# Kernel tuning notes

Hardware: AMD Instinct MI355X
Metric: run time of the kernel (lower is better)

The kernel has to match this reference:

```python
import jax, jax.numpy as jnp
import numpy as np

N_NODES = 100000
N_EDGES = 1000000
D = 64  # gat_input_size == gat_hidden_size
NEG_SLOPE = 0.2  # PyG GATConv default leaky_relu slope


def setup_inputs() -> dict:
    key = jax.random.key(0)
    k1, k2, k3, k4, k5, k6 = jax.random.split(key, 6)
    g = jax.random.normal(k1, (N_NODES, D), dtype=jnp.float32)
    edge_index = jax.random.randint(k2, (2, N_EDGES), 0, N_NODES, dtype=jnp.int32)
    scale = 1.0 / np.sqrt(D)
    W = jax.random.normal(k3, (D, D), dtype=jnp.float32) * scale
    att_src = jax.random.normal(k4, (D,), dtype=jnp.float32) * scale
    att_dst = jax.random.normal(k5, (D,), dtype=jnp.float32) * scale
    bias = jnp.zeros((D,), dtype=jnp.float32)
    return {"g": g, "edge_index": edge_index, "W": W,
            "att_src": att_src, "att_dst": att_dst, "bias": bias}


def _gat_layer(x, src, dst, W, att_src, att_dst, bias):
    N = x.shape[0]
    h = x @ W                               # [N, D] projected features
    a_src = h @ att_src                     # [N] per-node source logits
    a_dst = h @ att_dst                     # [N] per-node target logits
    e = jax.nn.leaky_relu(a_src[src] + a_dst[dst], NEG_SLOPE)  # [E]
    # numerically stable segment softmax over edges grouped by target node
    m = jax.ops.segment_max(e, dst, num_segments=N)            # [N]
    m = jnp.where(jnp.isfinite(m), m, 0.0)                     # isolated nodes
    ex = jnp.exp(e - m[dst])                                   # [E]
    denom = jax.ops.segment_sum(ex, dst, num_segments=N)       # [N]
    alpha = ex / (denom[dst] + 1e-16)                          # [E]
    out = jax.ops.segment_sum(alpha[:, None] * h[src], dst, num_segments=N)
    return out + bias


def reference(g, edge_index, W, att_src, att_dst, bias):
    src, dst = edge_index[0], edge_index[1]
    for _ in range(4):  # same shared GAT applied 4 times
        g = _gat_layer(g, src, dst, W, att_src, att_dst, bias)
    return g
```

## Files before the change

### kernel.cpp

```cpp
#include <hip/hip_runtime.h>
#include <hip/hip_bf16.h>

typedef unsigned int u32;
typedef unsigned short u16;
typedef unsigned long long u64;
typedef __attribute__((ext_vector_type(8))) short short8;
typedef __attribute__((ext_vector_type(4))) float f32x4;

#define LRELU_SLOPE 0.2f
#define BPB 32
#define MAXPER 13000

__device__ inline float bfbits(u32 hi) { union { u32 i; float f; } v; v.i = hi; return v.f; }
__device__ inline float bflo(u32 w) { return bfbits(w << 16); }
__device__ inline float bfhi(u32 w) { return bfbits(w & 0xFFFF0000u); }
__device__ inline float bf2f(u16 s) { return bfbits(((u32)s) << 16); }
__device__ inline u16 f2bf(float f) {
  union { float f; u32 i; } v; v.f = f;
  u32 r = v.i + 0x7FFFu + ((v.i >> 16) & 1u);
  return (u16)(r >> 16);
}

__global__ void detect_kernel(const u32* __restrict__ g, int nwords, int* __restrict__ mode) {
  __shared__ int cnt;
  if (threadIdx.x == 0) cnt = 0;
  __syncthreads();
  int c = 0;
  for (int i = threadIdx.x; i < nwords; i += blockDim.x) {
    u32 e = g[i] & 0x7F80u;
    if (e >= 0x3000u && e <= 0x4180u) c++;
  }
  atomicAdd(&cnt, c);
  __syncthreads();
  if (threadIdx.x == 0) *mode = (2 * cnt > nwords) ? 1 : 0;
}

__global__ void conv_x_kernel(const void* __restrict__ g, u16* __restrict__ x, int n,
                              const int* __restrict__ mode) {
  if (*mode) return;
  int i = blockIdx.x * blockDim.x + threadIdx.x;
  if (i >= n) return;
  x[i] = f2bf(((const float*)g)[i]);
}

__global__ void params_kernel(const void* __restrict__ W, const void* __restrict__ as,
                              const void* __restrict__ ad, const void* __restrict__ bs,
                              float* __restrict__ pf, u16* __restrict__ wfrag,
                              const int* __restrict__ mode) {
  int md = *mode;
  for (int i = threadIdx.x; i < 4288; i += 256) {
    const void* p; int j;
    if (i < 4096)      { p = W;  j = i; }
    else if (i < 4160) { p = as; j = i - 4096; }
    else if (i < 4224) { p = ad; j = i - 4160; }
    else               { p = bs; j = i - 4224; }
    pf[i] = md ? bf2f(((const u16*)p)[j]) : ((const float*)p)[j];
  }
  __syncthreads();
  for (int i = threadIdx.x; i < 4096; i += 256) {
    int f = i >> 9, lane = (i >> 3) & 63, j = i & 7;
    int c = f >> 1, t = f & 1;
    int k = 32 * t + 8 * (lane >> 4) + j;
    int n = 16 * c + (lane & 15);
    wfrag[i] = f2bf(pf[k * 64 + n]);
  }
}

__global__ void __launch_bounds__(256) binA_kernel(
    const int* __restrict__ src, const int* __restrict__ dst, int* __restrict__ gcnt,
    uint2* __restrict__ binned, int E, int nper, int cap) {
  __shared__ int lcnt[8], lbase[8], lcur[8];
  const int K = 8;
  int tile0 = blockIdx.x * (256 * K);
  int t = threadIdx.x;
  if (t < 8) { lcnt[t] = 0; lcur[t] = 0; }
  __syncthreads();
  int dv[K], sv[K], bv[K];
#pragma unroll
  for (int j = 0; j < K; ++j) {
    int idx = tile0 + j * 256 + t;
    bool ok = idx < E;
    int d = ok ? __builtin_nontemporal_load(&dst[idx]) : 0;
    int s = ok ? __builtin_nontemporal_load(&src[idx]) : 0;
    int b = -1;
    if (ok) {
      b = (d >= 4 * nper) ? 4 : 0;
      if (d >= (b + 2) * nper) b += 2;
      if (d >= (b + 1) * nper) b += 1;
      atomicAdd(&lcnt[b], 1);
    }
    dv[j] = d; sv[j] = s; bv[j] = b;
  }
  __syncthreads();
  if (t < 8) lbase[t] = atomicAdd(&gcnt[t], lcnt[t]);
  __syncthreads();
#pragma unroll
  for (int j = 0; j < K; ++j) {
    int b = bv[j];
    if (b >= 0) {
      int slot = lbase[b] + atomicAdd(&lcur[b], 1);
      if (slot < cap) binned[(size_t)b * cap + slot] = make_uint2((u32)sv[j], (u32)dv[j]);
    }
  }
}

__global__ void __launch_bounds__(256) histA_kernel(
    const uint2* __restrict__ binned, const int* __restrict__ gcnt,
    u32* __restrict__ slices, int nper, int cap) {
  __shared__ u32 cnt_lds[MAXPER];
  int b = blockIdx.x & 7;
  int j = blockIdx.x >> 3;
  int cnt = gcnt[b]; if (cnt > cap) cnt = cap;
  int chunk = (cnt + BPB - 1) / BPB;
  int begin = j * chunk;
  int endc = begin + chunk; if (endc > cnt) endc = cnt;
  for (int k = threadIdx.x; k < nper; k += 256) cnt_lds[k] = 0;
  __syncthreads();
  const uint2* reg = binned + (size_t)b * cap;
  int kbase = b * nper;
  for (int i = begin + threadIdx.x; i < endc; i += 256)
    atomicAdd(&cnt_lds[(int)reg[i].y - kbase], 1u);
  __syncthreads();
  u32* out = slices + (size_t)(b * BPB + j) * nper;
  for (int k = threadIdx.x; k < nper; k += 256) out[k] = cnt_lds[k];
}

__global__ void reduce_deg_kernel(const u32* __restrict__ slices, int* __restrict__ deg,
                                  int nper, int N) {
  int b = blockIdx.x & 7;
  int kk = (blockIdx.x >> 3) * blockDim.x + threadIdx.x;
  if (kk >= nper) return;
  int k = b * nper + kk;
  if (k >= N) return;
  const u32* s = slices + (size_t)b * BPB * nper + kk;
  u32 t = 0;
#pragma unroll 8
  for (int j = 0; j < BPB; ++j) t += s[(size_t)j * nper];
  deg[k] = (int)t;
}

__global__ void base_kernel(u32* __restrict__ slices, const int* __restrict__ row_off,
                            int nper, int N) {
  int b = blockIdx.x & 7;
  int kk = (blockIdx.x >> 3) * blockDim.x + threadIdx.x;
  if (kk >= nper) return;
  int k = b * nper + kk;
  if (k >= N) return;
  u32 run = (u32)row_off[k];
  u32* s = slices + (size_t)b * BPB * nper + kk;
#pragma unroll 8
  for (int j = 0; j < BPB; ++j) {
    u32 t = s[(size_t)j * nper];
    s[(size_t)j * nper] = run;
    run += t;
  }
}

__global__ void __launch_bounds__(256) scatterB_kernel(
    const uint2* __restrict__ binned, const int* __restrict__ gcnt,
    const u32* __restrict__ slices, int* __restrict__ csr_src, int nper, int cap) {
  __shared__ u32 base_lds[MAXPER];
  int b = blockIdx.x & 7;
  int j = blockIdx.x >> 3;
  int cnt = gcnt[b]; if (cnt > cap) cnt = cap;
  int chunk = (cnt + BPB - 1) / BPB;
  int begin = j * chunk;
  int endc = begin + chunk; if (endc > cnt) endc = cnt;
  const u32* s = slices + (size_t)(b * BPB + j) * nper;
  for (int k = threadIdx.x; k < nper; k += 256) base_lds[k] = s[k];
  __syncthreads();
  const uint2* reg = binned + (size_t)b * cap;
  int kbase = b * nper;
  for (int i = begin + threadIdx.x; i < endc; i += 256) {
    uint2 r = reg[i];
    u32 p = atomicAdd(&base_lds[(int)r.y - kbase], 1u);
    csr_src[p] = (int)r.x;
  }
}

__global__ void hist_local_kernel(const uint2* __restrict__ binned, const int* __restrict__ gcnt,
                                  int* __restrict__ deg, int cap) {
  int b = blockIdx.x & 7;
  int vb = blockIdx.x >> 3, nvb = gridDim.x >> 3;
  int cnt = gcnt[b]; if (cnt > cap) cnt = cap;
  const uint2* reg = binned + (size_t)b * cap;
  for (int i = vb * blockDim.x + threadIdx.x; i < cnt; i += nvb * blockDim.x)
    atomicAdd(&deg[reg[i].y], 1);
}

__global__ void scatter_local_kernel(const uint2* __restrict__ binned, const int* __restrict__ gcnt,
                                     int* __restrict__ cursor, int* __restrict__ csr_src, int cap) {
  int b = blockIdx.x & 7;
  int vb = blockIdx.x >> 3, nvb = gridDim.x >> 3;
  int cnt = gcnt[b]; if (cnt > cap) cnt = cap;
  const uint2* reg = binned + (size_t)b * cap;
  for (int i = vb * blockDim.x + threadIdx.x; i < cnt; i += nvb * blockDim.x) {
    uint2 r = reg[i];
    int p = atomicAdd(&cursor[r.y], 1);
    csr_src[p] = (int)r.x;
  }
}

__global__ void scan1_kernel(const int* __restrict__ deg, int* __restrict__ row_off,
                             int* __restrict__ partials, int N) {
  __shared__ int smem[1024];
  int t = threadIdx.x;
  int idx = blockIdx.x * 1024 + t;
  int v = (idx < N) ? deg[idx] : 0;
  smem[t] = v;
  __syncthreads();
  for (int off = 1; off < 1024; off <<= 1) {
    int u = (t >= off) ? smem[t - off] : 0;
    __syncthreads();
    smem[t] += u;
    __syncthreads();
  }
  if (idx < N) row_off[idx + 1] = smem[t];
  if (t == 1023) partials[blockIdx.x] = smem[t];
}

__global__ void scan2_kernel(int* __restrict__ partials, int P) {
  __shared__ int smem[1024];
  int t = threadIdx.x;
  int v = (t < P) ? partials[t] : 0;
  smem[t] = v;
  __syncthreads();
  for (int off = 1; off < 1024; off <<= 1) {
    int u = (t >= off) ? smem[t - off] : 0;
    __syncthreads();
    smem[t] += u;
    __syncthreads();
  }
  if (t < P) partials[t] = smem[t];
}

__global__ void scan3_kernel(int* __restrict__ row_off, const int* __restrict__ partials,
                             int* __restrict__ cursor, int N) {
  int b = blockIdx.x;
  int idx = b * 1024 + threadIdx.x;
  if (idx < N) {
    int v = row_off[idx + 1] + ((b > 0) ? partials[b - 1] : 0);
    row_off[idx + 1] = v;
    if (idx + 1 < N) cursor[idx + 1] = v;
  }
  if (idx == 0) { row_off[0] = 0; cursor[0] = 0; }
}

__global__ void __launch_bounds__(256) proj_mfma_kernel(
    const u16* __restrict__ x, const void* __restrict__ graw, const int* __restrict__ mode,
    int first, const u16* __restrict__ wfrag, const float* __restrict__ pf,
    u16* __restrict__ h, float* __restrict__ a_src, float* __restrict__ a_dst, int N) {
  int lane = threadIdx.x & 63;
  int quad = lane >> 4, m = lane & 15;
  int wtile = (int)((blockIdx.x * (size_t)blockDim.x + threadIdx.x) >> 6);
  int ntiles = (N + 15) >> 4;
  int nwaves = (int)((gridDim.x * (size_t)blockDim.x) >> 6);

  const u16* xin = (first && *mode) ? (const u16*)graw : x;

  short8 bfrag[8];
#pragma unroll
  for (int f = 0; f < 8; ++f)
    bfrag[f] = *(const short8*)(wfrag + f * 512 + lane * 8);
  float asv[4], adv[4];
#pragma unroll
  for (int c = 0; c < 4; ++c) {
    asv[c] = pf[4096 + 16 * c + m];
    adv[c] = pf[4160 + 16 * c + m];
  }

  for (int tile = wtile; tile < ntiles; tile += nwaves) {
    int row0 = tile << 4;
    int rl = row0 + m; if (rl > N - 1) rl = N - 1;
    const u16* xr = xin + (size_t)rl * 64 + 8 * quad;
    short8 a0 = *(const short8*)(xr);
    short8 a1 = *(const short8*)(xr + 32);

    f32x4 acc[4];
#pragma unroll
    for (int c = 0; c < 4; ++c) {
      f32x4 z = {0.f, 0.f, 0.f, 0.f};
      z = __builtin_amdgcn_mfma_f32_16x16x32_bf16(a0, bfrag[2 * c + 0], z, 0, 0, 0);
      z = __builtin_amdgcn_mfma_f32_16x16x32_bf16(a1, bfrag[2 * c + 1], z, 0, 0, 0);
      acc[c] = z;
    }

#pragma unroll
    for (int r = 0; r < 4; ++r) {
      int row = row0 + 4 * quad + r;
      float v0 = acc[0][r], v1 = acc[1][r], v2 = acc[2][r], v3 = acc[3][r];
      if (row < N) {
        u16* hr = h + (size_t)row * 64 + m;
        hr[0]  = f2bf(v0);
        hr[16] = f2bf(v1);
        hr[32] = f2bf(v2);
        hr[48] = f2bf(v3);
      }
      float s1 = v0 * asv[0] + v1 * asv[1] + v2 * asv[2] + v3 * asv[3];
      float s2 = v0 * adv[0] + v1 * adv[1] + v2 * adv[2] + v3 * adv[3];
#pragma unroll
      for (int msk = 1; msk <= 8; msk <<= 1) {
        s1 += __shfl_xor(s1, msk, 64);
        s2 += __shfl_xor(s2, msk, 64);
      }
      if (m == 0 && row < N) { a_src[row] = s1; a_dst[row] = s2; }
    }
  }
}

__global__ void __launch_bounds__(256) gather_kernel(
    const u16* __restrict__ h, const float* __restrict__ a_src,
    const float* __restrict__ a_dst, const int* __restrict__ row_off,
    const int* __restrict__ csr_src, const float* __restrict__ pf,
    u16* __restrict__ xout, void* __restrict__ dout, int N, int last,
    const int* __restrict__ mode) {
  int lane = threadIdx.x & 63;
  int grp = lane >> 4;
  int eg  = (lane >> 3) & 1;
  int fg  = lane & 7;
  int wid = (int)((blockIdx.x * blockDim.x + threadIdx.x) >> 6);
  int i0 = wid * 4;
  if (i0 >= N) return;
  int i = i0 + grp;
  bool valid = i < N;

  int beg = 0, end = 0;
  float adv = 0.f;
  if (valid) {
    beg = row_off[i];
    end = row_off[i + 1];
    adv = a_dst[i];
  }

  float acc[8] = {0.f, 0.f, 0.f, 0.f, 0.f, 0.f, 0.f, 0.f};
  float den = 0.f;

  if (beg < end) {
    int lastE = end - 1;
    for (int b0 = beg; b0 < end; b0 += 4) {
      int eA = b0 + eg;
      int eB = b0 + 2 + eg;
      float vA = (eA < end) ? 1.f : 0.f;
      float vB = (eB < end) ? 1.f : 0.f;
      int sA = csr_src[(eA < end) ? eA : lastE];
      int sB = csr_src[(eB < end) ? eB : lastE];
      float aA = a_src[sA];
      float aB = a_src[sB];
      uint4 hA = ((const uint4*)(h + (size_t)sA * 64))[fg];
      uint4 hB = ((const uint4*)(h + (size_t)sB * 64))[fg];

      float tA = aA + adv;
      tA = (tA > 0.f) ? tA : LRELU_SLOPE * tA;
      float wA = __expf(fminf(tA, 60.f)) * vA;
      float tB = aB + adv;
      tB = (tB > 0.f) ? tB : LRELU_SLOPE * tB;
      float wB = __expf(fminf(tB, 60.f)) * vB;
      den += wA + wB;
      acc[0] += wA * bflo(hA.x) + wB * bflo(hB.x);
      acc[1] += wA * bfhi(hA.x) + wB * bfhi(hB.x);
      acc[2] += wA * bflo(hA.y) + wB * bflo(hB.y);
      acc[3] += wA * bfhi(hA.y) + wB * bfhi(hB.y);
      acc[4] += wA * bflo(hA.z) + wB * bflo(hB.z);
      acc[5] += wA * bfhi(hA.z) + wB * bfhi(hB.z);
      acc[6] += wA * bflo(hA.w) + wB * bflo(hB.w);
      acc[7] += wA * bfhi(hA.w) + wB * bfhi(hB.w);
    }
  }

  den += __shfl_xor(den, 8, 64);
#pragma unroll
  for (int j = 0; j < 8; ++j) acc[j] += __shfl_xor(acc[j], 8, 64);
  float inv = (den > 0.f) ? 1.f / den : 0.f;

  if (!valid || eg) return;

  if (*mode || !last) {
    u32 o[4];
#pragma unroll
    for (int j = 0; j < 4; ++j) {
      float f0 = acc[2 * j]     * inv + pf[4224 + 8 * fg + 2 * j];
      float f1 = acc[2 * j + 1] * inv + pf[4224 + 8 * fg + 2 * j + 1];
      o[j] = (u32)f2bf(f0) | ((u32)f2bf(f1) << 16);
    }
    u16* base = last ? (u16*)dout : xout;
    *(uint4*)(base + (size_t)i * 64 + fg * 8) = make_uint4(o[0], o[1], o[2], o[3]);
  } else {
    float o[8];
#pragma unroll
    for (int j = 0; j < 8; ++j)
      o[j] = acc[j] * inv + pf[4224 + 8 * fg + j];
    float* dp = (float*)dout + (size_t)i * 64 + fg * 8;
    *(float4*)(dp)     = make_float4(o[0], o[1], o[2], o[3]);
    *(float4*)(dp + 4) = make_float4(o[4], o[5], o[6], o[7]);
  }
}

extern "C" void kernel_launch(void* const* d_in, const int* in_sizes, int n_in,
                              void* d_out, int out_size, void* d_ws, size_t ws_size,
                              hipStream_t stream) {
  const void* g     = d_in[0];
  const int*  edge  = (const int*)d_in[1];
  const void* Wp    = d_in[2];
  const void* attsp = d_in[3];
  const void* attdp = d_in[4];
  const void* biasp = d_in[5];

  const int D = 64;
  const int N = in_sizes[0] / D;
  const int E = in_sizes[1] / 2;
  const int* src = edge;
  const int* dst = edge + E;

  int nper = (N + 7) / 8;
  bool fast_csr = (nper <= MAXPER);

  char* ws = (char*)d_ws;
  size_t off = 0;
  auto alloc = [&](size_t bytes) -> char* {
    char* p = ws + off;
    off += (bytes + 255) & ~size_t(255);
    return p;
  };
  size_t h_bytes = (size_t)N * D * sizeof(u16);
  size_t slice_bytes = (size_t)8 * BPB * nper * sizeof(u32);
  u16*   x        = (u16*)alloc((size_t)N * D * sizeof(u16));
  u16*   h        = (u16*)alloc(h_bytes > slice_bytes ? h_bytes : slice_bytes);
  u32*   slices   = (u32*)h;
  float* pf       = (float*)alloc(4288 * sizeof(float));
  u16*   wfrag    = (u16*)alloc(4096 * sizeof(u16));
  float* a_src    = (float*)alloc((size_t)N * sizeof(float));
  float* a_dst    = (float*)alloc((size_t)N * sizeof(float));
  int*   deg      = (int*)alloc((size_t)N * sizeof(int));
  int*   row_off  = (int*)alloc((size_t)(N + 1) * sizeof(int));
  int*   cursor   = (int*)alloc((size_t)N * sizeof(int));
  int*   csr_src  = (int*)alloc((size_t)E * sizeof(int));
  int*   partials = (int*)alloc(1024 * sizeof(int));
  int*   mode     = (int*)alloc(256);
  int*   gcnt     = (int*)alloc(256);
  int    cap      = E / 8 + 16384;
  uint2* binned   = (uint2*)alloc((size_t)8 * cap * sizeof(uint2));

  detect_kernel<<<1, 256, 0, stream>>>((const u32*)g, 4096, mode);

  int n64 = N * D;
  conv_x_kernel<<<(n64 + 255) / 256, 256, 0, stream>>>(g, x, n64, mode);
  params_kernel<<<1, 256, 0, stream>>>(Wp, attsp, attdp, biasp, pf, wfrag, mode);

  hipMemsetAsync(gcnt, 0, 8 * sizeof(int), stream);
  if (!fast_csr) hipMemsetAsync(deg, 0, (size_t)N * sizeof(int), stream);
  int abl = (E + 2047) / 2048;
  binA_kernel<<<abl, 256, 0, stream>>>(src, dst, gcnt, binned, E, nper, cap);

  int nblk = (N + 1023) / 1024;
  if (fast_csr) {
    int kb = (nper + 255) / 256;
    histA_kernel<<<8 * BPB, 256, 0, stream>>>(binned, gcnt, slices, nper, cap);
    reduce_deg_kernel<<<8 * kb, 256, 0, stream>>>(slices, deg, nper, N);
    scan1_kernel<<<nblk, 1024, 0, stream>>>(deg, row_off, partials, N);
    scan2_kernel<<<1, 1024, 0, stream>>>(partials, nblk);
    scan3_kernel<<<nblk, 1024, 0, stream>>>(row_off, partials, cursor, N);
    base_kernel<<<8 * kb, 256, 0, stream>>>(slices, row_off, nper, N);
    scatterB_kernel<<<8 * BPB, 256, 0, stream>>>(binned, gcnt, slices, csr_src, nper, cap);
  } else {
    hist_local_kernel<<<1024, 256, 0, stream>>>(binned, gcnt, deg, cap);
    scan1_kernel<<<nblk, 1024, 0, stream>>>(deg, row_off, partials, N);
    scan2_kernel<<<1, 1024, 0, stream>>>(partials, nblk);
    scan3_kernel<<<nblk, 1024, 0, stream>>>(row_off, partials, cursor, N);
    scatter_local_kernel<<<1024, 256, 0, stream>>>(binned, gcnt, cursor, csr_src, cap);
  }

  int ntiles = (N + 15) / 16;
  int tblocks = (ntiles + 3) / 4;
  for (int layer = 0; layer < 4; ++layer) {
    proj_mfma_kernel<<<tblocks, 256, 0, stream>>>(x, g, mode, layer == 0 ? 1 : 0,
                                                  wfrag, pf, h, a_src, a_dst, N);
    int last = (layer == 3) ? 1 : 0;
    gather_kernel<<<(N + 15) / 16, 256, 0, stream>>>(h, a_src, a_dst, row_off, csr_src, pf,
                                                     x, d_out, N, last, mode);
  }
}
```

Measured before the change: 309.6 us.

## Fuse setup kernels, merge degree reduce into scan, unroll gather to 8 edges

Result: no change. 311.8 us (+0.7%).

```diff
diff --git a/kernel.cpp b/kernel.cpp
--- a/kernel.cpp
+++ b/kernel.cpp
@@ -21,33 +21,23 @@
   return (u16)(r >> 16);
 }
 
-__global__ void detect_kernel(const u32* __restrict__ g, int nwords, int* __restrict__ mode) {
+__global__ void dp_kernel(const u32* __restrict__ g, int nwords, int* __restrict__ mode,
+                          const void* __restrict__ W, const void* __restrict__ as,
+                          const void* __restrict__ ad, const void* __restrict__ bs,
+                          float* __restrict__ pf, u16* __restrict__ wfrag) {
   __shared__ int cnt;
   if (threadIdx.x == 0) cnt = 0;
   __syncthreads();
   int c = 0;
-  for (int i = threadIdx.x; i < nwords; i += blockDim.x) {
+  for (int i = threadIdx.x; i < nwords; i += 256) {
     u32 e = g[i] & 0x7F80u;
     if (e >= 0x3000u && e <= 0x4180u) c++;
   }
   atomicAdd(&cnt, c);
   __syncthreads();
-  if (threadIdx.x == 0) *mode = (2 * cnt > nwords) ? 1 : 0;
-}
-
-__global__ void conv_x_kernel(const void* __restrict__ g, u16* __restrict__ x, int n,
-                              const int* __restrict__ mode) {
-  if (*mode) return;
-  int i = blockIdx.x * blockDim.x + threadIdx.x;
-  if (i >= n) return;
-  x[i] = f2bf(((const float*)g)[i]);
-}
-
-__global__ void params_kernel(const void* __restrict__ W, const void* __restrict__ as,
-                              const void* __restrict__ ad, const void* __restrict__ bs,
-                              float* __restrict__ pf, u16* __restrict__ wfrag,
-                              const int* __restrict__ mode) {
-  int md = *mode;
+  int md = (2 * cnt > nwords) ? 1 : 0;
+  if (threadIdx.x == 0) *mode = md;
+
   for (int i = threadIdx.x; i < 4288; i += 256) {
     const void* p; int j;
     if (i < 4096)      { p = W;  j = i; }
@@ -59,11 +49,19 @@
   __syncthreads();
   for (int i = threadIdx.x; i < 4096; i += 256) {
     int f = i >> 9, lane = (i >> 3) & 63, j = i & 7;
-    int c = f >> 1, t = f & 1;
+    int cc = f >> 1, t = f & 1;
     int k = 32 * t + 8 * (lane >> 4) + j;
-    int n = 16 * c + (lane & 15);
+    int n = 16 * cc + (lane & 15);
     wfrag[i] = f2bf(pf[k * 64 + n]);
   }
+}
+
+__global__ void conv_x_kernel(const void* __restrict__ g, u16* __restrict__ x, int n,
+                              const int* __restrict__ mode) {
+  if (*mode) return;
+  int stride = gridDim.x * blockDim.x;
+  for (int i = blockIdx.x * blockDim.x + threadIdx.x; i < n; i += stride)
+    x[i] = f2bf(((const float*)g)[i]);
 }
 
 __global__ void __launch_bounds__(256) binA_kernel(
@@ -125,34 +123,66 @@
   for (int k = threadIdx.x; k < nper; k += 256) out[k] = cnt_lds[k];
 }
 
-__global__ void reduce_deg_kernel(const u32* __restrict__ slices, int* __restrict__ deg,
-                                  int nper, int N) {
-  int b = blockIdx.x & 7;
-  int kk = (blockIdx.x >> 3) * blockDim.x + threadIdx.x;
-  if (kk >= nper) return;
-  int k = b * nper + kk;
-  if (k >= N) return;
-  const u32* s = slices + (size_t)b * BPB * nper + kk;
-  u32 t = 0;
+__global__ void scan1f_kernel(const u32* __restrict__ slices, int* __restrict__ row_off,
+                              int* __restrict__ partials, int nper, int N) {
+  __shared__ int smem[1024];
+  int t = threadIdx.x;
+  int idx = blockIdx.x * 1024 + t;
+  int v = 0;
+  if (idx < N) {
+    int b = idx / nper;
+    int kk = idx - b * nper;
+    const u32* s = slices + (size_t)b * BPB * nper + kk;
+    u32 tt = 0;
 #pragma unroll 8
-  for (int j = 0; j < BPB; ++j) t += s[(size_t)j * nper];
-  deg[k] = (int)t;
-}
-
-__global__ void base_kernel(u32* __restrict__ slices, const int* __restrict__ row_off,
-                            int nper, int N) {
-  int b = blockIdx.x & 7;
-  int kk = (blockIdx.x >> 3) * blockDim.x + threadIdx.x;
-  if (kk >= nper) return;
-  int k = b * nper + kk;
-  if (k >= N) return;
-  u32 run = (u32)row_off[k];
-  u32* s = slices + (size_t)b * BPB * nper + kk;
+    for (int j = 0; j < BPB; ++j) tt += s[(size_t)j * nper];
+    v = (int)tt;
+  }
+  smem[t] = v;
+  __syncthreads();
+  for (int off = 1; off < 1024; off <<= 1) {
+    int u = (t >= off) ? smem[t - off] : 0;
+    __syncthreads();
+    smem[t] += u;
+    __syncthreads();
+  }
+  if (idx < N) row_off[idx + 1] = smem[t];
+  if (t == 1023) partials[blockIdx.x] = smem[t];
+}
+
+__global__ void scan2_kernel(int* __restrict__ partials, int P) {
+  __shared__ int smem[1024];
+  int t = threadIdx.x;
+  int v = (t < P) ? partials[t] : 0;
+  smem[t] = v;
+  __syncthreads();
+  for (int off = 1; off < 1024; off <<= 1) {
+    int u = (t >= off) ? smem[t - off] : 0;
+    __syncthreads();
+    smem[t] += u;
+    __syncthreads();
+  }
+  if (t < P) partials[t] = smem[t];
+}
+
+__global__ void scan3b_kernel(int* __restrict__ row_off, const int* __restrict__ partials,
+                              u32* __restrict__ slices, int nper, int N) {
+  int blk = blockIdx.x;
+  int idx = blk * 1024 + threadIdx.x;
+  if (idx == 0) row_off[0] = 0;
+  if (idx < N) {
+    int v = row_off[idx + 1] + ((blk > 0) ? partials[blk - 1] : 0);
+    row_off[idx + 1] = v;
+    int b = idx / nper;
+    int kk = idx - b * nper;
+    u32* s = slices + (size_t)b * BPB * nper + kk;
+    u32 run = (u32)v;
 #pragma unroll 8
-  for (int j = 0; j < BPB; ++j) {
-    u32 t = s[(size_t)j * nper];
-    s[(size_t)j * nper] = run;
-    run += t;
+    for (int j = BPB - 1; j >= 0; --j) {
+      u32 tt = s[(size_t)j * nper];
+      run -= tt;
+      s[(size_t)j * nper] = run;
+    }
   }
 }
 
@@ -217,21 +247,6 @@
   }
   if (idx < N) row_off[idx + 1] = smem[t];
   if (t == 1023) partials[blockIdx.x] = smem[t];
-}
-
-__global__ void scan2_kernel(int* __restrict__ partials, int P) {
-  __shared__ int smem[1024];
-  int t = threadIdx.x;
-  int v = (t < P) ? partials[t] : 0;
-  smem[t] = v;
-  __syncthreads();
-  for (int off = 1; off < 1024; off <<= 1) {
-    int u = (t >= off) ? smem[t - off] : 0;
-    __syncthreads();
-    smem[t] += u;
-    __syncthreads();
-  }
-  if (t < P) partials[t] = smem[t];
 }
 
 __global__ void scan3_kernel(int* __restrict__ row_off, const int* __restrict__ partials,
@@ -337,33 +352,45 @@
 
   if (beg < end) {
     int lastE = end - 1;
-    for (int b0 = beg; b0 < end; b0 += 4) {
+    for (int b0 = beg; b0 < end; b0 += 8) {
       int eA = b0 + eg;
       int eB = b0 + 2 + eg;
+      int eC = b0 + 4 + eg;
+      int eD = b0 + 6 + eg;
       float vA = (eA < end) ? 1.f : 0.f;
       float vB = (eB < end) ? 1.f : 0.f;
+      float vC = (eC < end) ? 1.f : 0.f;
+      float vD = (eD < end) ? 1.f : 0.f;
       int sA = csr_src[(eA < end) ? eA : lastE];
       int sB = csr_src[(eB < end) ? eB : lastE];
+      int sC = csr_src[(eC < end) ? eC : lastE];
+      int sD = csr_src[(eD < end) ? eD : lastE];
       float aA = a_src[sA];
       float aB = a_src[sB];
+      float aC = a_src[sC];
+      float aD = a_src[sD];
       uint4 hA = ((const uint4*)(h + (size_t)sA * 64))[fg];
       uint4 hB = ((const uint4*)(h + (size_t)sB * 64))[fg];
-
-      float tA = aA + adv;
-      tA = (tA > 0.f) ? tA : LRELU_SLOPE * tA;
+      uint4 hC = ((const uint4*)(h + (size_t)sC * 64))[fg];
+      uint4 hD = ((const uint4*)(h + (size_t)sD * 64))[fg];
+
+      float tA = aA + adv; tA = (tA > 0.f) ? tA : LRELU_SLOPE * tA;
+      float tB = aB + adv; tB = (tB > 0.f) ? tB : LRELU_SLOPE * tB;
+      float tC = aC + adv; tC = (tC > 0.f) ? tC : LRELU_SLOPE * tC;
+      float tD = aD + adv; tD = (tD > 0.f) ? tD : LRELU_SLOPE * tD;
       float wA = __expf(fminf(tA, 60.f)) * vA;
-      float tB = aB + adv;
-      tB = (tB > 0.f) ? tB : LRELU_SLOPE * tB;
       float wB = __expf(fminf(tB, 60.f)) * vB;
-      den += wA + wB;
-      acc[0] += wA * bflo(hA.x) + wB * bflo(hB.x);
-      acc[1] += wA * bfhi(hA.x) + wB * bfhi(hB.x);
-      acc[2] += wA * bflo(hA.y) + wB * bflo(hB.y);
-      acc[3] += wA * bfhi(hA.y) + wB * bfhi(hB.y);
-      acc[4] += wA * bflo(hA.z) + wB * bflo(hB.z);
-      acc[5] += wA * bfhi(hA.z) + wB * bfhi(hB.z);
-      acc[6] += wA * bflo(hA.w) + wB * bflo(hB.w);
-      acc[7] += wA * bfhi(hA.w) + wB * bfhi(hB.w);
+      float wC = __expf(fminf(tC, 60.f)) * vC;
+      float wD = __expf(fminf(tD, 60.f)) * vD;
+      den += (wA + wB) + (wC + wD);
+      acc[0] += wA * bflo(hA.x) + wB * bflo(hB.x) + wC * bflo(hC.x) + wD * bflo(hD.x);
+      acc[1] += wA * bfhi(hA.x) + wB * bfhi(hB.x) + wC * bfhi(hC.x) + wD * bfhi(hD.x);
+      acc[2] += wA * bflo(hA.y) + wB * bflo(hB.y) + wC * bflo(hC.y) + wD * bflo(hD.y);
+      acc[3] += wA * bfhi(hA.y) + wB * bfhi(hB.y) + wC * bfhi(hC.y) + wD * bfhi(hD.y);
+      acc[4] += wA * bflo(hA.z) + wB * bflo(hB.z) + wC * bflo(hC.z) + wD * bflo(hD.z);
+      acc[5] += wA * bfhi(hA.z) + wB * bfhi(hB.z) + wC * bfhi(hC.z) + wD * bfhi(hD.z);
+      acc[6] += wA * bflo(hA.w) + wB * bflo(hB.w) + wC * bflo(hC.w) + wD * bflo(hD.w);
+      acc[7] += wA * bfhi(hA.w) + wB * bfhi(hB.w) + wC * bfhi(hC.w) + wD * bfhi(hD.w);
     }
   }
 
@@ -440,11 +467,12 @@
   int    cap      = E / 8 + 16384;
   uint2* binned   = (uint2*)alloc((size_t)8 * cap * sizeof(uint2));
 
-  detect_kernel<<<1, 256, 0, stream>>>((const u32*)g, 4096, mode);
+  dp_kernel<<<1, 256, 0, stream>>>((const u32*)g, 4096, mode, Wp, attsp, attdp, biasp,
+                                   pf, wfrag);
 
   int n64 = N * D;
-  conv_x_kernel<<<(n64 + 255) / 256, 256, 0, stream>>>(g, x, n64, mode);
-  params_kernel<<<1, 256, 0, stream>>>(Wp, attsp, attdp, biasp, pf, wfrag, mode);
+  int cblocks = (n64 + 255) / 256; if (cblocks > 2048) cblocks = 2048;
+  conv_x_kernel<<<cblocks, 256, 0, stream>>>(g, x, n64, mode);
 
   hipMemsetAsync(gcnt, 0, 8 * sizeof(int), stream);
   if (!fast_csr) hipMemsetAsync(deg, 0, (size_t)N * sizeof(int), stream);
@@ -453,13 +481,10 @@
 
   int nblk = (N + 1023) / 1024;
   if (fast_csr) {
-    int kb = (nper + 255) / 256;
     histA_kernel<<<8 * BPB, 256, 0, stream>>>(binned, gcnt, slices, nper, cap);
-    reduce_deg_kernel<<<8 * kb, 256, 0, stream>>>(slices, deg, nper, N);
-    scan1_kernel<<<nblk, 1024, 0, stream>>>(deg, row_off, partials, N);
+    scan1f_kernel<<<nblk, 1024, 0, stream>>>(slices, row_off, partials, nper, N);
     scan2_kernel<<<1, 1024, 0, stream>>>(partials, nblk);
-    scan3_kernel<<<nblk, 1024, 0, stream>>>(row_off, partials, cursor, N);
-    base_kernel<<<8 * kb, 256, 0, stream>>>(slices, row_off, nper, N);
+    scan3b_kernel<<<nblk, 1024, 0, stream>>>(row_off, partials, slices, nper, N);
     scatterB_kernel<<<8 * BPB, 256, 0, stream>>>(binned, gcnt, slices, csr_src, nper, cap);
   } else {
     hist_local_kernel<<<1024, 256, 0, stream>>>(binned, gcnt, deg, cap);
```
